# Kernel optimization log

Hardware: AMD Instinct MI355X
Metric: run time of the kernel (lower is better)

## Reference

```python
import jax, jax.numpy as jnp
import numpy as np

N_NODES = 100000
N_EDGES = 50000
NNZ = 1600000
D_IN = 128
D_OUT = 128  # heads(8) * out_channels(16)


def setup_inputs() -> dict:
    key = jax.random.key(0)
    k1, k2, k3, k4 = jax.random.split(key, 4)
    X = jax.random.normal(k1, (N_NODES, D_IN), dtype=jnp.float32)
    W = jax.random.normal(k2, (D_IN, D_OUT), dtype=jnp.float32) * (1.0 / np.sqrt(D_IN))
    eps = jnp.zeros((1,), dtype=jnp.float32)
    vertex = jax.random.randint(k3, (NNZ,), 0, N_NODES, dtype=jnp.int32)
    edges = jax.random.randint(k4, (NNZ,), 0, N_EDGES, dtype=jnp.int32)
    return {"X": X, "W": W, "eps": eps, "vertex": vertex, "edges": edges,
            "num_edges": N_EDGES}


def reference(X, W, eps, vertex, edges, num_edges):
    N = X.shape[0]
    Xp = X @ W                                   # [N, D_OUT] linear proj (no bias)
    Xve = Xp[vertex]                             # [nnz, D_OUT] vertex -> incidence gather
    Xe = jax.ops.segment_sum(Xve, edges, num_segments=num_edges)   # [E, D_OUT] first_aggregate='sum'
    Xev = Xe[edges]                              # [nnz, D_OUT] edge -> incidence gather
    Xv = jax.ops.segment_sum(Xev, vertex, num_segments=N)          # [N, D_OUT]
    out = (1.0 + eps) * Xp + Xv                  # GIN combine with learnable eps (eps is [1], broadcasts)
    return jax.nn.gelu(out, approximate=False)   # torch F.gelu default = exact erf
```

## Files before the change

### kernel.cpp

```cpp
#include <hip/hip_runtime.h>
#include <math.h>

#define NN 100000
#define NE 50000
#define NSEG (NE + NN)
#define DD 128

#define NBE 196
#define NBV 391
#define NB  (NBE + NBV)
#define CAP_E 8960
#define CAP_V 4608

static __device__ __forceinline__ float gelu_exact(float x) {
  return 0.5f * x * (1.0f + erff(x * 0.70710678118654752f));
}

static __device__ __forceinline__ int bucket_base(int g) {
  return (g < NBE) ? g * CAP_E : NBE * CAP_E + (g - NBE) * CAP_V;
}

static __device__ __forceinline__ void acc_bf16x2(float& a0, float& a1, unsigned u) {
  union { unsigned i; float f; } lo, hi;
  lo.i = u << 16;
  hi.i = u & 0xFFFF0000u;
  a0 += lo.f;
  a1 += hi.f;
}

static __device__ __forceinline__ unsigned pack_bf16x2(float a, float b) {
  unsigned ua = __float_as_uint(a), ub = __float_as_uint(b);
  ua = (ua + 0x7FFFu + ((ua >> 16) & 1u)) >> 16;
  ub = (ub + 0x7FFFu + ((ub >> 16) & 1u)) >> 16;
  return ua | (ub << 16);
}

__global__ void k_zero(int* __restrict__ gcur) {
  int g = blockIdx.x * blockDim.x + threadIdx.x;
  if (g < NB) gcur[g] = bucket_base(g);
}

__global__ __launch_bounds__(256) void k_gemm(const float* __restrict__ X,
                                              const float* __restrict__ W,
                                              float* __restrict__ Xp,
                                              unsigned* __restrict__ Xb2) {
  __shared__ float Xs[64 * 128];
  const int tid = threadIdx.x;
  const int rowbase = blockIdx.x * 64;
  const float4* __restrict__ X4 = (const float4*)X;
  float4* Xs4 = (float4*)Xs;
#pragma unroll
  for (int j = 0; j < 8; ++j) {
    int f = tid + j * 256;
    int row = rowbase + (f >> 5);
    float4 v = make_float4(0.f, 0.f, 0.f, 0.f);
    if (row < NN) v = X4[rowbase * 32 + f];
    Xs4[f] = v;
  }
  __syncthreads();
  const int cg = tid & 31;
  const int rg = tid >> 5;
  const float4* __restrict__ W4 = (const float4*)W;
  float4 acc[8];
#pragma unroll
  for (int r = 0; r < 8; ++r) acc[r] = make_float4(0.f, 0.f, 0.f, 0.f);
  for (int kb = 0; kb < 32; ++kb) {
    float4 w0 = W4[(4 * kb + 0) * 32 + cg];
    float4 w1 = W4[(4 * kb + 1) * 32 + cg];
    float4 w2 = W4[(4 * kb + 2) * 32 + cg];
    float4 w3 = W4[(4 * kb + 3) * 32 + cg];
#pragma unroll
    for (int r = 0; r < 8; ++r) {
      float4 xv = *(const float4*)&Xs[(rg * 8 + r) * 128 + 4 * kb];
      acc[r].x = fmaf(xv.x, w0.x, fmaf(xv.y, w1.x, fmaf(xv.z, w2.x, fmaf(xv.w, w3.x, acc[r].x))));
      acc[r].y = fmaf(xv.x, w0.y, fmaf(xv.y, w1.y, fmaf(xv.z, w2.y, fmaf(xv.w, w3.y, acc[r].y))));
      acc[r].z = fmaf(xv.x, w0.z, fmaf(xv.y, w1.z, fmaf(xv.z, w2.z, fmaf(xv.w, w3.z, acc[r].z))));
      acc[r].w = fmaf(xv.x, w0.w, fmaf(xv.y, w1.w, fmaf(xv.z, w2.w, fmaf(xv.w, w3.w, acc[r].w))));
    }
  }
#pragma unroll
  for (int r = 0; r < 8; ++r) {
    int row = rowbase + rg * 8 + r;
    if (row < NN) {
      ((float4*)Xp)[row * 32 + cg] = acc[r];
      uint2 p;
      p.x = pack_bf16x2(acc[r].x, acc[r].y);
      p.y = pack_bf16x2(acc[r].z, acc[r].w);
      ((uint2*)Xb2)[row * 32 + cg] = p;
    }
  }
}

__global__ __launch_bounds__(256) void k_pass1(const int* __restrict__ vertex,
                                               const int* __restrict__ edges,
                                               int* __restrict__ gcur,
                                               int* __restrict__ S, int nnz) {
  __shared__ int hist[NB];
  const int tid = threadIdx.x;
  for (int b = tid; b < NB; b += 256) hist[b] = 0;
  __syncthreads();
  const int base = blockIdx.x * 4096;
#pragma unroll
  for (int k = 0; k < 16; ++k) {
    int i = base + tid + k * 256;
    if (i < nnz) {
      atomicAdd(&hist[edges[i] >> 8], 1);
      atomicAdd(&hist[NBE + (vertex[i] >> 8)], 1);
    }
  }
  __syncthreads();
  for (int b = tid; b < NB; b += 256) {
    int c = hist[b];
    hist[b] = c ? atomicAdd(&gcur[b], c) : 0;
  }
  __syncthreads();
#pragma unroll
  for (int k = 0; k < 16; ++k) {
    int i = base + tid + k * 256;
    if (i < nnz) {
      int e = edges[i], v = vertex[i];
      int pe = atomicAdd(&hist[e >> 8], 1);
      S[pe] = ((e & 255) << 17) | v;
      int pv = atomicAdd(&hist[NBE + (v >> 8)], 1);
      S[pv] = ((v & 255) << 17) | e;
    }
  }
}

__global__ __launch_bounds__(1024) void k_bscan(const int* __restrict__ gcur,
                                                int* __restrict__ gbase) {
  __shared__ int s[1024];
  const int g = threadIdx.x;
  int cnt = 0;
  if (g < NB) cnt = gcur[g] - bucket_base(g);
  s[g] = cnt;
  __syncthreads();
  for (int off = 1; off < 1024; off <<= 1) {
    int y = (g >= off) ? s[g - off] : 0;
    __syncthreads();
    s[g] += y;
    __syncthreads();
  }
  if (g < NB) gbase[g] = s[g] - cnt;
}

__global__ __launch_bounds__(256) void k_pass2(const int* __restrict__ gcur,
                                               const int* __restrict__ gbase,
                                               const int* __restrict__ S,
                                               int* __restrict__ L,
                                               int* __restrict__ O) {
  __shared__ int offs[257];
  __shared__ int cur[256];
  __shared__ int scratch[CAP_E];
  const int g = blockIdx.x;
  const int tid = threadIdx.x;
  const bool isE = g < NBE;
  const int sstart = bucket_base(g);
  int nit = gcur[g] - sstart;
  const int cap = isE ? CAP_E : CAP_V;
  if (nit > cap) nit = cap;
  const int s0 = isE ? (g << 8) : ((g - NBE) << 8);
  const int segN = min(256, (isE ? NE : NN) - s0);
  const int obase = isE ? s0 : NE + s0;
  const int dbase = gbase[g];
  for (int k = tid; k < 257; k += 256) offs[k] = 0;
  __syncthreads();
  for (int t = tid; t < nit; t += 256) atomicAdd(&offs[(S[sstart + t] >> 17) + 1], 1);
  __syncthreads();
  for (int off = 1; off < 256; off <<= 1) {
    int y = (tid >= off) ? offs[tid + 1 - off] : 0;
    __syncthreads();
    offs[tid + 1] += y;
    __syncthreads();
  }
  cur[tid] = offs[tid];
  __syncthreads();
  for (int t = tid; t < nit; t += 256) {
    int u = S[sstart + t];
    int r = atomicAdd(&cur[u >> 17], 1);
    scratch[r] = u & 0x1FFFF;
  }
  __syncthreads();
  for (int t = tid; t < nit; t += 256) L[dbase + t] = scratch[t];
  for (int k = tid; k <= segN; k += 256) O[obase + k] = dbase + offs[k];
}

__global__ __launch_bounds__(256) void k_edge_agg(const unsigned* __restrict__ Xb2,
                                                  const int* __restrict__ O,
                                                  const int* __restrict__ L,
                                                  unsigned* __restrict__ Xe2) {
  const int e = blockIdx.x * 4 + (threadIdx.x >> 6);
  const int lane = threadIdx.x & 63;
  const int q = lane >> 4;
  const int ql = lane & 15;
  const int start = O[e];
  const int end = O[e + 1];
  const uint4* __restrict__ P = (const uint4*)Xb2;
  float a[8];
#pragma unroll
  for (int k = 0; k < 8; ++k) a[k] = 0.f;
  int j = start + q;
  for (; j + 4 < end; j += 8) {
    uint4 u0 = P[L[j] * 16 + ql];
    uint4 u1 = P[L[j + 4] * 16 + ql];
    acc_bf16x2(a[0], a[1], u0.x); acc_bf16x2(a[2], a[3], u0.y);
    acc_bf16x2(a[4], a[5], u0.z); acc_bf16x2(a[6], a[7], u0.w);
    acc_bf16x2(a[0], a[1], u1.x); acc_bf16x2(a[2], a[3], u1.y);
    acc_bf16x2(a[4], a[5], u1.z); acc_bf16x2(a[6], a[7], u1.w);
  }
  if (j < end) {
    uint4 u0 = P[L[j] * 16 + ql];
    acc_bf16x2(a[0], a[1], u0.x); acc_bf16x2(a[2], a[3], u0.y);
    acc_bf16x2(a[4], a[5], u0.z); acc_bf16x2(a[6], a[7], u0.w);
  }
#pragma unroll
  for (int k = 0; k < 8; ++k) {
    a[k] += __shfl_xor(a[k], 16);
    a[k] += __shfl_xor(a[k], 32);
  }
  if (q == 0) {
    uint4 o;
    o.x = pack_bf16x2(a[0], a[1]);
    o.y = pack_bf16x2(a[2], a[3]);
    o.z = pack_bf16x2(a[4], a[5]);
    o.w = pack_bf16x2(a[6], a[7]);
    ((uint4*)Xe2)[e * 16 + ql] = o;
  }
}

__global__ __launch_bounds__(256) void k_vert_agg(const unsigned* __restrict__ Xe2,
                                                  const int* __restrict__ O,
                                                  const int* __restrict__ L,
                                                  const float* __restrict__ eps,
                                                  float* __restrict__ XpOut) {
  const int v = blockIdx.x * 4 + (threadIdx.x >> 6);
  const int lane = threadIdx.x & 63;
  const int q = lane >> 4;
  const int ql = lane & 15;
  const int start = O[NE + v];
  const int end = O[NE + v + 1];
  const uint4* __restrict__ Q = (const uint4*)Xe2;
  float a[8];
#pragma unroll
  for (int k = 0; k < 8; ++k) a[k] = 0.f;
  int j = start + q;
  for (; j + 4 < end; j += 8) {
    uint4 u0 = Q[L[j] * 16 + ql];
    uint4 u1 = Q[L[j + 4] * 16 + ql];
    acc_bf16x2(a[0], a[1], u0.x); acc_bf16x2(a[2], a[3], u0.y);
    acc_bf16x2(a[4], a[5], u0.z); acc_bf16x2(a[6], a[7], u0.w);
    acc_bf16x2(a[0], a[1], u1.x); acc_bf16x2(a[2], a[3], u1.y);
    acc_bf16x2(a[4], a[5], u1.z); acc_bf16x2(a[6], a[7], u1.w);
  }
  if (j < end) {
    uint4 u0 = Q[L[j] * 16 + ql];
    acc_bf16x2(a[0], a[1], u0.x); acc_bf16x2(a[2], a[3], u0.y);
    acc_bf16x2(a[4], a[5], u0.z); acc_bf16x2(a[6], a[7], u0.w);
  }
#pragma unroll
  for (int k = 0; k < 8; ++k) {
    a[k] += __shfl_xor(a[k], 16);
    a[k] += __shfl_xor(a[k], 32);
  }
  if (q == 0) {
    float4* P2 = (float4*)XpOut;
    float4 x0 = P2[v * 32 + ql * 2];
    float4 x1 = P2[v * 32 + ql * 2 + 1];
    float s = 1.0f + eps[0];
    x0.x = gelu_exact(fmaf(s, x0.x, a[0]));
    x0.y = gelu_exact(fmaf(s, x0.y, a[1]));
    x0.z = gelu_exact(fmaf(s, x0.z, a[2]));
    x0.w = gelu_exact(fmaf(s, x0.w, a[3]));
    x1.x = gelu_exact(fmaf(s, x1.x, a[4]));
    x1.y = gelu_exact(fmaf(s, x1.y, a[5]));
    x1.z = gelu_exact(fmaf(s, x1.z, a[6]));
    x1.w = gelu_exact(fmaf(s, x1.w, a[7]));
    P2[v * 32 + ql * 2] = x0;
    P2[v * 32 + ql * 2 + 1] = x1;
  }
}

extern "C" void kernel_launch(void* const* d_in, const int* in_sizes, int n_in,
                              void* d_out, int out_size, void* d_ws, size_t ws_size,
                              hipStream_t stream) {
  const float* X = (const float*)d_in[0];
  const float* W = (const float*)d_in[1];
  const float* eps = (const float*)d_in[2];
  const int* vertex = (const int*)d_in[3];
  const int* edges = (const int*)d_in[4];
  const int nnz = in_sizes[3];

  char* ws = (char*)d_ws;
  size_t off = 0;
  auto alloc = [&](size_t bytes) -> void* {
    void* p = ws + off;
    off = (off + bytes + 255) & ~(size_t)255;
    return p;
  };
  const size_t stagingB = ((size_t)NBE * CAP_E + (size_t)NBV * CAP_V) * 4;
  const size_t xbB = (size_t)NN * DD * 2;
  void* A = alloc(xbB > stagingB ? xbB : stagingB);
  int* S = (int*)A;
  unsigned* Xb2 = (unsigned*)A;
  unsigned* Xe2 = (unsigned*)alloc((size_t)NE * DD * 2);
  int* L = (int*)alloc((size_t)2 * nnz * sizeof(int));
  int* O = (int*)alloc((size_t)(NSEG + 1) * sizeof(int));
  int* gcur = (int*)alloc((size_t)NB * sizeof(int));
  int* gbase = (int*)alloc((size_t)NB * sizeof(int));
  if (off > ws_size) return;

  float* Xp = (float*)d_out;

  k_zero<<<3, 256, 0, stream>>>(gcur);
  k_pass1<<<(nnz + 4095) / 4096, 256, 0, stream>>>(vertex, edges, gcur, S, nnz);
  k_bscan<<<1, 1024, 0, stream>>>(gcur, gbase);
  k_pass2<<<NB, 256, 0, stream>>>(gcur, gbase, S, L, O);
  k_gemm<<<(NN + 63) / 64, 256, 0, stream>>>(X, W, Xp, Xb2);
  k_edge_agg<<<NE / 4, 256, 0, stream>>>(Xb2, O, L, Xe2);
  k_vert_agg<<<NN / 4, 256, 0, stream>>>(Xe2, O, L, eps, Xp);
}
```

Baseline: 336.6 us.

## Use bf16 MFMA for projection GEMM and spread aggregation epilogue across lanes

Replaces the FP32 shared-memory FMA GEMM with bf16 MFMA 16x16x32 instructions. A small new kernel pre-transposes W to bf16, and X is converted to bf16 on load. The edge and vertex aggregation kernels now write their final reduction from all 64 lanes with interleaved feature ownership instead of only the q==0 lanes. This also turns the epilogue writes into narrower scattered stores (scalar float and short per element in the GEMM). The precision of the projection drops to bf16 inputs, which adds numerical risk.

```diff
diff --git a/kernel.cpp b/kernel.cpp
--- a/kernel.cpp
+++ b/kernel.cpp
@@ -12,6 +12,10 @@
 #define CAP_E 8960
 #define CAP_V 4608
 
+typedef short bf16x8 __attribute__((ext_vector_type(8)));
+typedef float f32x4 __attribute__((ext_vector_type(4)));
+typedef float v2f __attribute__((ext_vector_type(2)));
+
 static __device__ __forceinline__ float gelu_exact(float x) {
   return 0.5f * x * (1.0f + erff(x * 0.70710678118654752f));
 }
@@ -20,12 +24,14 @@
   return (g < NBE) ? g * CAP_E : NBE * CAP_E + (g - NBE) * CAP_V;
 }
 
-static __device__ __forceinline__ void acc_bf16x2(float& a0, float& a1, unsigned u) {
+static __device__ __forceinline__ void acc2(v2f& a, unsigned u) {
   union { unsigned i; float f; } lo, hi;
   lo.i = u << 16;
   hi.i = u & 0xFFFF0000u;
-  a0 += lo.f;
-  a1 += hi.f;
+  v2f t;
+  t.x = lo.f;
+  t.y = hi.f;
+  a += t;
 }
 
 static __device__ __forceinline__ unsigned pack_bf16x2(float a, float b) {
@@ -35,58 +41,74 @@
   return ua | (ub << 16);
 }
 
+static __device__ __forceinline__ unsigned short bf16_rne(float a) {
+  unsigned ua = __float_as_uint(a);
+  ua = (ua + 0x7FFFu + ((ua >> 16) & 1u)) >> 16;
+  return (unsigned short)ua;
+}
+
 __global__ void k_zero(int* __restrict__ gcur) {
   int g = blockIdx.x * blockDim.x + threadIdx.x;
   if (g < NB) gcur[g] = bucket_base(g);
 }
 
+__global__ void k_wt(const float* __restrict__ W, unsigned short* __restrict__ Wt) {
+  int idx = blockIdx.x * 256 + threadIdx.x;
+  int k = idx >> 7, n = idx & 127;
+  Wt[n * 128 + k] = bf16_rne(W[idx]);
+}
+
 __global__ __launch_bounds__(256) void k_gemm(const float* __restrict__ X,
-                                              const float* __restrict__ W,
+                                              const unsigned short* __restrict__ Wt,
                                               float* __restrict__ Xp,
-                                              unsigned* __restrict__ Xb2) {
-  __shared__ float Xs[64 * 128];
+                                              unsigned short* __restrict__ Xb2) {
   const int tid = threadIdx.x;
-  const int rowbase = blockIdx.x * 64;
+  const int w = tid >> 6;
+  const int l = tid & 63;
+  const int lm = l & 15;
+  const int lk = l >> 4;
+  const int R = blockIdx.x * 64 + w * 16;
+  const int arow = R + lm;
+  const bool rowok = arow < NN;
   const float4* __restrict__ X4 = (const float4*)X;
-  float4* Xs4 = (float4*)Xs;
-#pragma unroll
-  for (int j = 0; j < 8; ++j) {
-    int f = tid + j * 256;
-    int row = rowbase + (f >> 5);
-    float4 v = make_float4(0.f, 0.f, 0.f, 0.f);
-    if (row < NN) v = X4[rowbase * 32 + f];
-    Xs4[f] = v;
-  }
-  __syncthreads();
-  const int cg = tid & 31;
-  const int rg = tid >> 5;
-  const float4* __restrict__ W4 = (const float4*)W;
-  float4 acc[8];
-#pragma unroll
-  for (int r = 0; r < 8; ++r) acc[r] = make_float4(0.f, 0.f, 0.f, 0.f);
-  for (int kb = 0; kb < 32; ++kb) {
-    float4 w0 = W4[(4 * kb + 0) * 32 + cg];
-    float4 w1 = W4[(4 * kb + 1) * 32 + cg];
-    float4 w2 = W4[(4 * kb + 2) * 32 + cg];
-    float4 w3 = W4[(4 * kb + 3) * 32 + cg];
-#pragma unroll
-    for (int r = 0; r < 8; ++r) {
-      float4 xv = *(const float4*)&Xs[(rg * 8 + r) * 128 + 4 * kb];
-      acc[r].x = fmaf(xv.x, w0.x, fmaf(xv.y, w1.x, fmaf(xv.z, w2.x, fmaf(xv.w, w3.x, acc[r].x))));
-      acc[r].y = fmaf(xv.x, w0.y, fmaf(xv.y, w1.y, fmaf(xv.z, w2.y, fmaf(xv.w, w3.y, acc[r].y))));
-      acc[r].z = fmaf(xv.x, w0.z, fmaf(xv.y, w1.z, fmaf(xv.z, w2.z, fmaf(xv.w, w3.z, acc[r].z))));
-      acc[r].w = fmaf(xv.x, w0.w, fmaf(xv.y, w1.w, fmaf(xv.z, w2.w, fmaf(xv.w, w3.w, acc[r].w))));
-    }
-  }
-#pragma unroll
-  for (int r = 0; r < 8; ++r) {
-    int row = rowbase + rg * 8 + r;
+  const uint4* __restrict__ Wt4 = (const uint4*)Wt;
+
+  f32x4 acc[8];
+#pragma unroll
+  for (int t = 0; t < 8; ++t) acc[t] = (f32x4)(0.f);
+
+  for (int c = 0; c < 4; ++c) {
+    const int k0 = c * 32 + lk * 8;
+    float4 x0 = make_float4(0.f, 0.f, 0.f, 0.f), x1 = x0;
+    if (rowok) {
+      x0 = X4[arow * 32 + (k0 >> 2)];
+      x1 = X4[arow * 32 + (k0 >> 2) + 1];
+    }
+    union { bf16x8 v; uint4 u; } a;
+    a.u.x = pack_bf16x2(x0.x, x0.y);
+    a.u.y = pack_bf16x2(x0.z, x0.w);
+    a.u.z = pack_bf16x2(x1.x, x1.y);
+    a.u.w = pack_bf16x2(x1.z, x1.w);
+#pragma unroll
+    for (int t = 0; t < 8; ++t) {
+      union { bf16x8 v; uint4 u; } b;
+      b.u = Wt4[(t * 16 + lm) * 16 + c * 4 + lk];
+      acc[t] = __builtin_amdgcn_mfma_f32_16x16x32_bf16(a.v, b.v, acc[t], 0, 0, 0);
+    }
+  }
+
+  const int drow = R + lk * 4;
+#pragma unroll
+  for (int r = 0; r < 4; ++r) {
+    const int row = drow + r;
     if (row < NN) {
-      ((float4*)Xp)[row * 32 + cg] = acc[r];
-      uint2 p;
-      p.x = pack_bf16x2(acc[r].x, acc[r].y);
-      p.y = pack_bf16x2(acc[r].z, acc[r].w);
-      ((uint2*)Xb2)[row * 32 + cg] = p;
+#pragma unroll
+      for (int t = 0; t < 8; ++t) {
+        const float v = acc[t][r];
+        const int col = t * 16 + lm;
+        Xp[row * 128 + col] = v;
+        Xb2[row * 128 + col] = bf16_rne(v);
+      }
     }
   }
 }
@@ -196,36 +218,30 @@
   const int start = O[e];
   const int end = O[e + 1];
   const uint4* __restrict__ P = (const uint4*)Xb2;
-  float a[8];
-#pragma unroll
-  for (int k = 0; k < 8; ++k) a[k] = 0.f;
+  v2f a[4];
+#pragma unroll
+  for (int k = 0; k < 4; ++k) a[k] = (v2f)(0.f);
   int j = start + q;
   for (; j + 4 < end; j += 8) {
     uint4 u0 = P[L[j] * 16 + ql];
     uint4 u1 = P[L[j + 4] * 16 + ql];
-    acc_bf16x2(a[0], a[1], u0.x); acc_bf16x2(a[2], a[3], u0.y);
-    acc_bf16x2(a[4], a[5], u0.z); acc_bf16x2(a[6], a[7], u0.w);
-    acc_bf16x2(a[0], a[1], u1.x); acc_bf16x2(a[2], a[3], u1.y);
-    acc_bf16x2(a[4], a[5], u1.z); acc_bf16x2(a[6], a[7], u1.w);
+    acc2(a[0], u0.x); acc2(a[1], u0.y); acc2(a[2], u0.z); acc2(a[3], u0.w);
+    acc2(a[0], u1.x); acc2(a[1], u1.y); acc2(a[2], u1.z); acc2(a[3], u1.w);
   }
   if (j < end) {
     uint4 u0 = P[L[j] * 16 + ql];
-    acc_bf16x2(a[0], a[1], u0.x); acc_bf16x2(a[2], a[3], u0.y);
-    acc_bf16x2(a[4], a[5], u0.z); acc_bf16x2(a[6], a[7], u0.w);
-  }
-#pragma unroll
-  for (int k = 0; k < 8; ++k) {
-    a[k] += __shfl_xor(a[k], 16);
-    a[k] += __shfl_xor(a[k], 32);
-  }
-  if (q == 0) {
-    uint4 o;
-    o.x = pack_bf16x2(a[0], a[1]);
-    o.y = pack_bf16x2(a[2], a[3]);
-    o.z = pack_bf16x2(a[4], a[5]);
-    o.w = pack_bf16x2(a[6], a[7]);
-    ((uint4*)Xe2)[e * 16 + ql] = o;
-  }
+    acc2(a[0], u0.x); acc2(a[1], u0.y); acc2(a[2], u0.z); acc2(a[3], u0.w);
+  }
+#pragma unroll
+  for (int k = 0; k < 4; ++k) {
+    float u0 = a[k].x, u1 = a[k].y;
+    u0 += __shfl_xor(u0, 16); u0 += __shfl_xor(u0, 32);
+    u1 += __shfl_xor(u1, 16); u1 += __shfl_xor(u1, 32);
+    a[k].x = u0; a[k].y = u1;
+  }
+  float s0 = (q == 0) ? a[0].x : (q == 1) ? a[1].x : (q == 2) ? a[2].x : a[3].x;
+  float s1 = (q == 0) ? a[0].y : (q == 1) ? a[1].y : (q == 2) ? a[2].y : a[3].y;
+  Xe2[e * 64 + ql * 4 + q] = pack_bf16x2(s0, s1);
 }
 
 __global__ __launch_bounds__(256) void k_vert_agg(const unsigned* __restrict__ Xe2,
@@ -240,44 +256,36 @@
   const int start = O[NE + v];
   const int end = O[NE + v + 1];
   const uint4* __restrict__ Q = (const uint4*)Xe2;
-  float a[8];
-#pragma unroll
-  for (int k = 0; k < 8; ++k) a[k] = 0.f;
+  v2f a[4];
+#pragma unroll
+  for (int k = 0; k < 4; ++k) a[k] = (v2f)(0.f);
   int j = start + q;
   for (; j + 4 < end; j += 8) {
     uint4 u0 = Q[L[j] * 16 + ql];
     uint4 u1 = Q[L[j + 4] * 16 + ql];
-    acc_bf16x2(a[0], a[1], u0.x); acc_bf16x2(a[2], a[3], u0.y);
-    acc_bf16x2(a[4], a[5], u0.z); acc_bf16x2(a[6], a[7], u0.w);
-    acc_bf16x2(a[0], a[1], u1.x); acc_bf16x2(a[2], a[3], u1.y);
-    acc_bf16x2(a[4], a[5], u1.z); acc_bf16x2(a[6], a[7], u1.w);
+    acc2(a[0], u0.x); acc2(a[1], u0.y); acc2(a[2], u0.z); acc2(a[3], u0.w);
+    acc2(a[0], u1.x); acc2(a[1], u1.y); acc2(a[2], u1.z); acc2(a[3], u1.w);
   }
   if (j < end) {
     uint4 u0 = Q[L[j] * 16 + ql];
-    acc_bf16x2(a[0], a[1], u0.x); acc_bf16x2(a[2], a[3], u0.y);
-    acc_bf16x2(a[4], a[5], u0.z); acc_bf16x2(a[6], a[7], u0.w);
-  }
-#pragma unroll
-  for (int k = 0; k < 8; ++k) {
-    a[k] += __shfl_xor(a[k], 16);
-    a[k] += __shfl_xor(a[k], 32);
-  }
-  if (q == 0) {
-    float4* P2 = (float4*)XpOut;
-    float4 x0 = P2[v * 32 + ql * 2];
-    float4 x1 = P2[v * 32 + ql * 2 + 1];
-    float s = 1.0f + eps[0];
-    x0.x = gelu_exact(fmaf(s, x0.x, a[0]));
-    x0.y = gelu_exact(fmaf(s, x0.y, a[1]));
-    x0.z = gelu_exact(fmaf(s, x0.z, a[2]));
-    x0.w = gelu_exact(fmaf(s, x0.w, a[3]));
-    x1.x = gelu_exact(fmaf(s, x1.x, a[4]));
-    x1.y = gelu_exact(fmaf(s, x1.y, a[5]));
-    x1.z = gelu_exact(fmaf(s, x1.z, a[6]));
-    x1.w = gelu_exact(fmaf(s, x1.w, a[7]));
-    P2[v * 32 + ql * 2] = x0;
-    P2[v * 32 + ql * 2 + 1] = x1;
-  }
+    acc2(a[0], u0.x); acc2(a[1], u0.y); acc2(a[2], u0.z); acc2(a[3], u0.w);
+  }
+#pragma unroll
+  for (int k = 0; k < 4; ++k) {
+    float u0 = a[k].x, u1 = a[k].y;
+    u0 += __shfl_xor(u0, 16); u0 += __shfl_xor(u0, 32);
+    u1 += __shfl_xor(u1, 16); u1 += __shfl_xor(u1, 32);
+    a[k].x = u0; a[k].y = u1;
+  }
+  float s0 = (q == 0) ? a[0].x : (q == 1) ? a[1].x : (q == 2) ? a[2].x : a[3].x;
+  float s1 = (q == 0) ? a[0].y : (q == 1) ? a[1].y : (q == 2) ? a[2].y : a[3].y;
+  float2* __restrict__ P2 = (float2*)XpOut;
+  const int fi = v * 64 + ql * 4 + q;
+  float2 x = P2[fi];
+  const float sc = 1.0f + eps[0];
+  x.x = gelu_exact(fmaf(sc, x.x, s0));
+  x.y = gelu_exact(fmaf(sc, x.y, s1));
+  P2[fi] = x;
 }
 
 extern "C" void kernel_launch(void* const* d_in, const int* in_sizes, int n_in,
@@ -301,21 +309,23 @@
   const size_t xbB = (size_t)NN * DD * 2;
   void* A = alloc(xbB > stagingB ? xbB : stagingB);
   int* S = (int*)A;
-  unsigned* Xb2 = (unsigned*)A;
+  unsigned short* Xb2 = (unsigned short*)A;
   unsigned* Xe2 = (unsigned*)alloc((size_t)NE * DD * 2);
   int* L = (int*)alloc((size_t)2 * nnz * sizeof(int));
   int* O = (int*)alloc((size_t)(NSEG + 1) * sizeof(int));
   int* gcur = (int*)alloc((size_t)NB * sizeof(int));
   int* gbase = (int*)alloc((size_t)NB * sizeof(int));
+  unsigned short* Wt = (unsigned short*)alloc((size_t)DD * DD * 2);
   if (off > ws_size) return;
 
   float* Xp = (float*)d_out;
 
   k_zero<<<3, 256, 0, stream>>>(gcur);
+  k_wt<<<64, 256, 0, stream>>>(W, Wt);
   k_pass1<<<(nnz + 4095) / 4096, 256, 0, stream>>>(vertex, edges, gcur, S, nnz);
   k_bscan<<<1, 1024, 0, stream>>>(gcur, gbase);
   k_pass2<<<NB, 256, 0, stream>>>(gcur, gbase, S, L, O);
-  k_gemm<<<(NN + 63) / 64, 256, 0, stream>>>(X, W, Xp, Xb2);
-  k_edge_agg<<<NE / 4, 256, 0, stream>>>(Xb2, O, L, Xe2);
+  k_gemm<<<(NN + 63) / 64, 256, 0, stream>>>(X, Wt, Xp, Xb2);
+  k_edge_agg<<<NE / 4, 256, 0, stream>>>((const unsigned*)Xb2, O, L, Xe2);
   k_vert_agg<<<NN / 4, 256, 0, stream>>>(Xe2, O, L, eps, Xp);
 }
```

Result: faster. 324.9 us (-3.4%).
